# Kernel tuning notes

Measured on AMD Instinct MI355X. Metric: run time of the kernel, lower is better.

Reference implementation:

```python
import jax, jax.numpy as jnp
import numpy as np

EXPERT_NUM = 8
SEQ_LEN = 4096
FREQ_LEN = SEQ_LEN // 2 + 1


def setup_inputs() -> dict:
    key = jax.random.key(0)
    ks = jax.random.split(key, 6)
    B, C = 32, 8
    x = jax.random.normal(ks[0], (B, C, SEQ_LEN), dtype=jnp.float32)
    raw = jax.random.uniform(ks[1], (EXPERT_NUM - 1,), dtype=jnp.float32)
    s1 = 1.0 / np.sqrt(FREQ_LEN)
    W1 = jax.random.uniform(ks[2], (FREQ_LEN, FREQ_LEN), jnp.float32, -s1, s1)
    b1 = jax.random.uniform(ks[3], (FREQ_LEN,), jnp.float32, -s1, s1)
    W2 = jax.random.uniform(ks[4], (EXPERT_NUM, FREQ_LEN), jnp.float32, -s1, s1)
    b2 = jax.random.uniform(ks[5], (EXPERT_NUM,), jnp.float32, -s1, s1)
    return {"x": x, "raw": raw, "W1": W1, "b1": b1, "W2": W2, "b2": b2}


def reference(x, raw, W1, b1, W2, b2):
    # instance norm over seq dim (unbiased variance, like torch.var default)
    x_mean = jnp.mean(x, axis=2, keepdims=True)
    xc = x - x_mean
    n = x.shape[2]
    x_var = jnp.sum(xc * xc, axis=2, keepdims=True) / (n - 1) + 1e-5
    xn = xc / jnp.sqrt(x_var)

    freq_x = jnp.fft.rfft(xn, axis=-1)            # [B, C, F] complex
    F_ = freq_x.shape[-1]

    # sorted sigmoid boundaries -> integer band edges (non-differentiable cast)
    b = jnp.sort(jax.nn.sigmoid(raw))
    boundaries = jnp.concatenate([jnp.zeros(1, x.dtype), b, jnp.ones(1, x.dtype)])
    idx = jnp.floor(jax.lax.stop_gradient(boundaries) * F_).astype(jnp.int32)
    idx = idx.at[-1].set(F_)

    # band-pass masks for all experts at once: [E, F]
    fpos = jnp.arange(F_)
    mask = (fpos[None, :] >= idx[:-1, None]) & (fpos[None, :] < idx[1:, None])

    # per-expert frequency components: [B, E, C, F]
    comp = freq_x[:, None, :, :] * mask[None, :, None, :].astype(freq_x.dtype)
    expert_outputs = jnp.fft.irfft(comp, n=SEQ_LEN, axis=-1)  # [B, E, C, L]

    # gating on channel-averaged magnitude spectrum
    gating_input = jnp.mean(jnp.abs(freq_x), axis=1)          # [B, F]
    h = jax.nn.relu(gating_input @ W1.T + b1)
    gating_scores = jax.nn.softmax(h @ W2.T + b2, axis=-1)    # [B, E]

    # gated combine in frequency domain, then single iFFT
    gate_c = gating_scores.astype(freq_x.dtype)
    combined_freq = jnp.einsum('becf,be->bcf', comp, gate_c)
    combined = jnp.fft.irfft(combined_freq, n=SEQ_LEN, axis=-1)
    combined = combined * jnp.sqrt(x_var) + x_mean
    return combined, boundaries, gating_scores, expert_outputs
```

## Files before the change

kernel.cpp:

```cpp
#include <hip/hip_runtime.h>
#include <hip/hip_bf16.h>


using cplx = float2;
typedef float nfloat2 __attribute__((ext_vector_type(2)));

static constexpr int BB = 32, CCH = 8, LL = 4096, FF = 2049, EE = 8;

static constexpr size_t WS_FREQ  = 0;
static constexpr size_t WS_MEAN  = WS_FREQ + (size_t)BB * CCH * FF * 2;
static constexpr size_t WS_SIGMA = WS_MEAN + 256;
static constexpr size_t WS_AMAG  = WS_SIGMA + 256;
static constexpr size_t WS_H     = WS_AMAG + (size_t)BB * CCH * FF;
static constexpr size_t WS_IDX   = WS_H + (size_t)BB * FF;
static constexpr size_t WS_EOF   = WS_IDX + 16;

static constexpr size_t OUT_COMB = 0;
static constexpr size_t OUT_BND  = (size_t)BB * CCH * LL;
static constexpr size_t OUT_GATE = OUT_BND + 9;
static constexpr size_t OUT_EXP  = OUT_GATE + (size_t)BB * EE;

__device__ float2 g_W2048[2048];
__device__ float2 g_U[2049];
__device__ int    g_tabcnt = 0;

#define PHI(i) ((i) + ((i) >> 5))
__device__ __forceinline__ int scat(int n) {
  return ((n & 3) << 9) | (((n >> 2) & 7) << 6) | (((n >> 5) & 7) << 3) | (n >> 8);
}

template <bool INV>
__device__ __forceinline__ void dft8(float* zr, float* zi) {
  const float C = 0.70710678118654752f;
  float s0r = zr[0] + zr[4], s0i = zi[0] + zi[4];
  float d0r = zr[0] - zr[4], d0i = zi[0] - zi[4];
  float s1r = zr[2] + zr[6], s1i = zi[2] + zi[6];
  float d1r = zr[2] - zr[6], d1i = zi[2] - zi[6];
  float E0r = s0r + s1r, E0i = s0i + s1i;
  float E2r = s0r - s1r, E2i = s0i - s1i;
  float E1r, E1i, E3r, E3i;
  if (!INV) { E1r = d0r + d1i; E1i = d0i - d1r; E3r = d0r - d1i; E3i = d0i + d1r; }
  else      { E1r = d0r - d1i; E1i = d0i + d1r; E3r = d0r + d1i; E3i = d0i - d1r; }
  float t0r = zr[1] + zr[5], t0i = zi[1] + zi[5];
  float e0r = zr[1] - zr[5], e0i = zi[1] - zi[5];
  float t1r = zr[3] + zr[7], t1i = zi[3] + zi[7];
  float e1r = zr[3] - zr[7], e1i = zi[3] - zi[7];
  float O0r = t0r + t1r, O0i = t0i + t1i;
  float O2r = t0r - t1r, O2i = t0i - t1i;
  float O1r, O1i, O3r, O3i;
  if (!INV) { O1r = e0r + e1i; O1i = e0i - e1r; O3r = e0r - e1i; O3i = e0i + e1r; }
  else      { O1r = e0r - e1i; O1i = e0i + e1r; O3r = e0r + e1i; O3i = e0i - e1r; }
  float w1r, w1i, w2r, w2i, w3r, w3i;
  if (!INV) {
    w1r = C * (O1r + O1i); w1i = C * (O1i - O1r);
    w2r = O2i;             w2i = -O2r;
    w3r = C * (O3i - O3r); w3i = -C * (O3r + O3i);
  } else {
    w1r = C * (O1r - O1i); w1i = C * (O1i + O1r);
    w2r = -O2i;            w2i = O2r;
    w3r = -C * (O3r + O3i); w3i = C * (O3r - O3i);
  }
  zr[0] = E0r + O0r; zi[0] = E0i + O0i;
  zr[4] = E0r - O0r; zi[4] = E0i - O0i;
  zr[1] = E1r + w1r; zi[1] = E1i + w1i;
  zr[5] = E1r - w1r; zi[5] = E1i - w1i;
  zr[2] = E2r + w2r; zi[2] = E2i + w2i;
  zr[6] = E2r - w2r; zi[6] = E2i - w2i;
  zr[3] = E3r + w3r; zi[3] = E3i + w3i;
  zr[7] = E3r - w3r; zi[7] = E3i - w3i;
}

template <bool INV>
__device__ __forceinline__ void dft4(float* zr, float* zi) {
  float s0r = zr[0] + zr[2], s0i = zi[0] + zi[2];
  float d0r = zr[0] - zr[2], d0i = zi[0] - zi[2];
  float s1r = zr[1] + zr[3], s1i = zi[1] + zi[3];
  float d1r = zr[1] - zr[3], d1i = zi[1] - zi[3];
  zr[0] = s0r + s1r; zi[0] = s0i + s1i;
  zr[2] = s0r - s1r; zi[2] = s0i - s1i;
  if (!INV) { zr[1] = d0r + d1i; zi[1] = d0i - d1r; zr[3] = d0r - d1i; zi[3] = d0i + d1r; }
  else      { zr[1] = d0r - d1i; zi[1] = d0i + d1r; zr[3] = d0r + d1i; zi[3] = d0i - d1r; }
}

template <bool INV>
__device__ void fftr8(float* ZR, float* ZI, const cplx* __restrict__ W, int t) {
  float zr[8], zi[8];
  {
    int base = 8 * t;
#pragma unroll
    for (int m = 0; m < 8; ++m) { int i = PHI(base + m); zr[m] = ZR[i]; zi[m] = ZI[i]; }
    dft8<INV>(zr, zi);
#pragma unroll
    for (int m = 0; m < 8; ++m) { int i = PHI(base + m); ZR[i] = zr[m]; ZI[i] = zi[m]; }
  }
  __syncthreads();
  {
    int g = t & 31, p = t >> 5;
    int base = 64 * g + p;
#pragma unroll
    for (int m = 0; m < 8; ++m) { int i = PHI(base + 8 * m); zr[m] = ZR[i]; zi[m] = ZI[i]; }
#pragma unroll
    for (int m = 1; m < 8; ++m) {
      cplx w = W[32 * m * p];
      float wi = INV ? -w.y : w.y;
      float xr = zr[m] * w.x - zi[m] * wi;
      float xi = zr[m] * wi + zi[m] * w.x;
      zr[m] = xr; zi[m] = xi;
    }
    dft8<INV>(zr, zi);
#pragma unroll
    for (int m = 0; m < 8; ++m) { int i = PHI(base + 8 * m); ZR[i] = zr[m]; ZI[i] = zi[m]; }
  }
  __syncthreads();
  {
    int g = t & 3, p = t >> 2;
    int base = 512 * g + p;
#pragma unroll
    for (int m = 0; m < 8; ++m) { int i = PHI(base + 64 * m); zr[m] = ZR[i]; zi[m] = ZI[i]; }
#pragma unroll
    for (int m = 1; m < 8; ++m) {
      cplx w = W[4 * m * p];
      float wi = INV ? -w.y : w.y;
      float xr = zr[m] * w.x - zi[m] * wi;
      float xi = zr[m] * wi + zi[m] * w.x;
      zr[m] = xr; zi[m] = xi;
    }
    dft8<INV>(zr, zi);
#pragma unroll
    for (int m = 0; m < 8; ++m) { int i = PHI(base + 64 * m); ZR[i] = zr[m]; ZI[i] = zi[m]; }
  }
  __syncthreads();
  {
#pragma unroll
    for (int h = 0; h < 2; ++h) {
      int p = t + (h << 8);
      float yr[4], yi[4];
#pragma unroll
      for (int m = 0; m < 4; ++m) { int i = PHI(p + 512 * m); yr[m] = ZR[i]; yi[m] = ZI[i]; }
#pragma unroll
      for (int m = 1; m < 4; ++m) {
        cplx w = W[m * p];
        float wi = INV ? -w.y : w.y;
        float xr = yr[m] * w.x - yi[m] * wi;
        float xi = yr[m] * wi + yi[m] * w.x;
        yr[m] = xr; yi[m] = xi;
      }
      dft4<INV>(yr, yi);
#pragma unroll
      for (int m = 0; m < 4; ++m) { int i = PHI(p + 512 * m); ZR[i] = yr[m]; ZI[i] = yi[m]; }
    }
  }
  __syncthreads();
}

__device__ __forceinline__ void expert_ifft(const float* __restrict__ ws,
                                            float* __restrict__ out,
                                            float* ZR, float* ZI,
                                            int bc, int j, int t) {
  const int b = bc >> 3, c = bc & 7;
  const cplx* freq = (const cplx*)ws + (size_t)bc * FF;
  const int*  idxp = (const int*)(ws + WS_IDX);
  const int lo = idxp[j], hi = idxp[j + 1];

#pragma unroll
  for (int u = 0; u < 8; ++u) {
    int k  = t + (u << 8);
    int km = 2048 - k;
    cplx A = make_float2(0.f, 0.f), Bv = make_float2(0.f, 0.f);
    if (k >= lo && k < hi)   A  = freq[k];
    if (km >= lo && km < hi) Bv = freq[km];
    float Px = A.x - Bv.x, Py = A.y + Bv.y;
    float Qx = A.x + Bv.x, Qy = A.y - Bv.y;
    cplx uk = g_U[k];
    float cs = uk.x, sn = -uk.y;
    float Xox = 0.5f * (cs * Px - sn * Py);
    float Xoy = 0.5f * (cs * Py + sn * Px);
    int i = PHI(scat(k));
    ZR[i] = 0.5f * Qx - Xoy;
    ZI[i] = 0.5f * Qy + Xox;
  }
  __syncthreads();

  fftr8<true>(ZR, ZI, g_W2048, t);

  const float mul = 1.0f / 2048.0f;
  float* op = out + OUT_EXP + (((size_t)(b * EE + j) * CCH + c) * LL);
  if (t == 0) __builtin_nontemporal_store(ZR[PHI(0)] * mul, op);
#pragma unroll
  for (int u = 0; u < 8; ++u) {
    int n = t + (u << 8);
    if (n < 2047) {
      nfloat2 o;
      o.x = ZI[PHI(n)] * mul;
      o.y = ZR[PHI(n + 1)] * mul;
      __builtin_nontemporal_store(o, (nfloat2*)(op + 2 * n + 1));
    } else {
      __builtin_nontemporal_store(ZI[PHI(2047)] * mul, op + 4095);
    }
  }
}

__global__ __launch_bounds__(256) void k_fwd(const float* __restrict__ x,
                                             const float* __restrict__ raw,
                                             float* __restrict__ ws,
                                             float* __restrict__ out) {
  const int p = blockIdx.x, t = threadIdx.x;

  if (p >= 256) {
    if (p < 273) {
      if (__hip_atomic_load(&g_tabcnt, __ATOMIC_RELAXED, __HIP_MEMORY_SCOPE_AGENT) < 17) {
        if (p < 264) {
          int jj = (p - 256) * 256 + t;
          float sn, cs;
          sincosf(-6.283185307179586f * (float)jj / 2048.0f, &sn, &cs);
          g_W2048[jj] = make_float2(cs, sn);
        } else {
          int k = (p - 264) * 256 + t;
          if (k < FF) {
            float sn, cs;
            sincosf(-3.14159265358979323846f * (float)k / 2048.0f, &sn, &cs);
            g_U[k] = make_float2(cs, sn);
          }
        }
        __syncthreads();
        if (t == 0) {
          __threadfence();
          __hip_atomic_fetch_add(&g_tabcnt, 1, __ATOMIC_RELEASE, __HIP_MEMORY_SCOPE_AGENT);
        }
      }
    } else if (p == 273) {
      __shared__ int idx_s[9];
      if (t == 0) {
        float v[7];
        for (int i = 0; i < 7; ++i) v[i] = 1.0f / (1.0f + expf(-raw[i]));
        for (int a = 1; a < 7; ++a) {
          float key = v[a];
          int q = a - 1;
          while (q >= 0 && v[q] > key) { v[q + 1] = v[q]; --q; }
          v[q + 1] = key;
        }
        float bnd[9];
        bnd[0] = 0.0f; bnd[8] = 1.0f;
        for (int i = 0; i < 7; ++i) bnd[i + 1] = v[i];
        int* wi = (int*)(ws + WS_IDX);
        for (int e = 0; e < 9; ++e) {
          int id = (int)floorf(bnd[e] * (float)FF);
          if (e == 8) id = FF;
          idx_s[e] = id;
          wi[e] = id;
          out[OUT_BND + e] = bnd[e];
        }
      }
      __syncthreads();
      int* eof = (int*)(ws + WS_EOF);
      for (int f = t; f < FF; f += 256) {
        int e = 0;
        for (int q = 1; q < 8; ++q)
          if (f >= idx_s[q]) e = q;
        eof[f] = e;
      }
    } else {
      float4* hp = (float4*)(ws + WS_H);
      const float4 z4 = make_float4(0.f, 0.f, 0.f, 0.f);
      for (int i = (p - 274) * 256 + t; i < 16392; i += 8 * 256) hp[i] = z4;
    }
    return;
  }

  __shared__ float ZR[2112], ZI[2112];
  __shared__ float red[8];
  const int bc = p;
  const int lane = t & 63, wid = t >> 6;
  const float2* xp2 = (const float2*)(x + (size_t)bc * LL);

  float2 v[8];
  float sum = 0.f;
#pragma unroll
  for (int u = 0; u < 8; ++u) {
    v[u] = xp2[t + (u << 8)];
    sum += v[u].x + v[u].y;
  }
#pragma unroll
  for (int off = 32; off > 0; off >>= 1) sum += __shfl_down(sum, off, 64);
  if (lane == 0) red[wid] = sum;
  __syncthreads();
  const float mean = (red[0] + red[1] + red[2] + red[3]) * (1.0f / 4096.0f);

  float ss = 0.f;
#pragma unroll
  for (int u = 0; u < 8; ++u) {
    float dx = v[u].x - mean, dy = v[u].y - mean;
    ss += dx * dx + dy * dy;
  }
#pragma unroll
  for (int off = 32; off > 0; off >>= 1) ss += __shfl_down(ss, off, 64);
  if (lane == 0) red[4 + wid] = ss;
  __syncthreads();
  const float var   = (red[4] + red[5] + red[6] + red[7]) / 4095.0f + 1e-5f;
  const float sigma = sqrtf(var);
  const float inv   = 1.0f / sigma;
  if (t == 0) {
    ws[WS_MEAN + bc]  = mean;
    ws[WS_SIGMA + bc] = sigma;
  }

#pragma unroll
  for (int u = 0; u < 8; ++u) {
    int n = t + (u << 8);
    int i = PHI(scat(n));
    ZR[i] = (v[u].x - mean) * inv;
    ZI[i] = (v[u].y - mean) * inv;
  }
  if (t == 0) {
    while (__hip_atomic_load(&g_tabcnt, __ATOMIC_ACQUIRE, __HIP_MEMORY_SCOPE_AGENT) < 17) {
      __builtin_amdgcn_s_sleep(8);
    }
  }
  __syncthreads();

  fftr8<false>(ZR, ZI, g_W2048, t);

  cplx* freq = (cplx*)ws + (size_t)bc * FF;
#pragma unroll
  for (int u = 0; u < 9; ++u) {
    int k = t + (u << 8);
    if (k > 2048) break;
    int ka = k & 2047, km = (2048 - k) & 2047;
    float Zkr = ZR[PHI(ka)], Zki = ZI[PHI(ka)];
    float Zmr = ZR[PHI(km)], Zmi = ZI[PHI(km)];
    float fex = 0.5f * (Zkr + Zmr);
    float fey = 0.5f * (Zki - Zmi);
    float fox = 0.5f * (Zki + Zmi);
    float foy = -0.5f * (Zkr - Zmr);
    cplx uk = g_U[k];
    float rx = fex + uk.x * fox - uk.y * foy;
    float ry = fey + uk.x * foy + uk.y * fox;
    freq[k] = make_float2(rx, ry);
    ws[WS_AMAG + (size_t)bc * FF + k] = 0.125f * sqrtf(rx * rx + ry * ry);
  }
}

__global__ __launch_bounds__(256) void k_mid(const float* __restrict__ W1,
                                             float* __restrict__ ws,
                                             float* __restrict__ out) {
  __shared__ float SM[4224];
  const int p = blockIdx.x, t = threadIdx.x;

  if (p < 1089) {
    float* W1s = SM;
    float* gis = SM + 2112;
    const int i0 = (p % 33) * 64;
    const int il = t & 63, bg = t >> 6;
    float acc[8] = {0, 0, 0, 0, 0, 0, 0, 0};
    const int fbeg = (p / 33) * 64;
    const int fend = min(fbeg + 64, FF);
    for (int f0 = fbeg; f0 < fend; f0 += 32) {
      for (int q = t; q < 64 * 32; q += 256) {
        int r = q >> 5, cc = q & 31;
        int gi_i = i0 + r, gf = f0 + cc;
        W1s[r * 33 + cc] = (gi_i < FF && gf < FF) ? W1[(size_t)gi_i * FF + gf] : 0.f;
      }
      for (int q = t; q < 32 * 32; q += 256) {
        int bb = q >> 5, cc = q & 31;
        int gf = f0 + cc;
        float s = 0.f;
        if (gf < FF) {
          const float* ap = ws + WS_AMAG + (size_t)(bb * 8) * FF + gf;
#pragma unroll
          for (int c = 0; c < 8; ++c) s += ap[(size_t)c * FF];
        }
        gis[bb * 33 + cc] = s;
      }
      __syncthreads();
#pragma unroll 8
      for (int cc = 0; cc < 32; ++cc) {
        float wv = W1s[il * 33 + cc];
#pragma unroll
        for (int j = 0; j < 8; ++j) acc[j] += wv * gis[(bg * 8 + j) * 33 + cc];
      }
      __syncthreads();
    }
    int ii = i0 + il;
    if (ii < FF) {
#pragma unroll
      for (int j = 0; j < 8; ++j)
        atomicAdd(&ws[WS_H + (size_t)(bg * 8 + j) * FF + ii], acc[j]);
    }
    return;
  }
  if (p < 1096) return;

  const int e   = p - 1096;
  const int xcd = e & 7, s = e >> 3;
  const int grp = s / 6, j = s % 6;
  const int bc  = (grp << 3) | xcd;

  expert_ifft(ws, out, SM, SM + 2112, bc, j, t);
}

__global__ __launch_bounds__(256) void k_comb(const float* __restrict__ b1,
                                              const float* __restrict__ W2,
                                              const float* __restrict__ b2,
                                              const float* __restrict__ ws,
                                              float* __restrict__ out) {
  __shared__ float ZR[2112], ZI[2112];
  const int p = blockIdx.x, t = threadIdx.x;

  if (p >= 256) {
    const int q  = p - 256;
    const int jj = q >> 8, bc = q & 255;
    expert_ifft(ws, out, ZR, ZI, bc, 6 + jj, t);
    return;
  }

  __shared__ float red[4][8];
  __shared__ float lg[8];
  __shared__ float gates_s[8];
  const int bc = p;
  const int b  = bc >> 3, c = bc & 7;
  const int lane = t & 63, wid = t >> 6;

  float pacc[8] = {0, 0, 0, 0, 0, 0, 0, 0};
  const float* hrow = ws + WS_H + (size_t)b * FF;
  for (int f = t; f < FF; f += 256) {
    float hv = fmaxf(hrow[f] + b1[f], 0.f);
#pragma unroll
    for (int e = 0; e < 8; ++e) pacc[e] += hv * W2[(size_t)e * FF + f];
  }
#pragma unroll
  for (int off = 32; off > 0; off >>= 1) {
#pragma unroll
    for (int e = 0; e < 8; ++e) pacc[e] += __shfl_down(pacc[e], off, 64);
  }
  if (lane == 0) {
#pragma unroll
    for (int e = 0; e < 8; ++e) red[wid][e] = pacc[e];
  }
  __syncthreads();
  if (t < 8) lg[t] = red[0][t] + red[1][t] + red[2][t] + red[3][t] + b2[t];
  __syncthreads();
  if (t < 8) {
    float mx = lg[0];
#pragma unroll
    for (int q = 1; q < 8; ++q) mx = fmaxf(mx, lg[q]);
    float sm = 0.f;
#pragma unroll
    for (int q = 0; q < 8; ++q) sm += expf(lg[q] - mx);
    float g = expf(lg[t] - mx) / sm;
    gates_s[t] = g;
    if (c == 0) out[OUT_GATE + (size_t)b * 8 + t] = g;
  }
  __syncthreads();

  const cplx* freq = (const cplx*)ws + (size_t)bc * FF;
  const int*  eof  = (const int*)(ws + WS_EOF);

#pragma unroll
  for (int u = 0; u < 8; ++u) {
    int k  = t + (u << 8);
    int km = 2048 - k;
    cplx A  = freq[k];
    cplx Bv = freq[km];
    float gk = gates_s[eof[k]], gm = gates_s[eof[km]];
    A.x *= gk; A.y *= gk; Bv.x *= gm; Bv.y *= gm;
    float Px = A.x - Bv.x, Py = A.y + Bv.y;
    float Qx = A.x + Bv.x, Qy = A.y - Bv.y;
    cplx uk = g_U[k];
    float cs = uk.x, sn = -uk.y;
    float Xox = 0.5f * (cs * Px - sn * Py);
    float Xoy = 0.5f * (cs * Py + sn * Px);
    int i = PHI(scat(k));
    ZR[i] = 0.5f * Qx - Xoy;
    ZI[i] = 0.5f * Qy + Xox;
  }
  __syncthreads();

  fftr8<true>(ZR, ZI, g_W2048, t);

  const float mul = ws[WS_SIGMA + bc] * (1.0f / 2048.0f);
  const float add = ws[WS_MEAN + bc];
  nfloat2* op = (nfloat2*)(out + OUT_COMB + (size_t)bc * LL);
#pragma unroll
  for (int u = 0; u < 8; ++u) {
    int n = t + (u << 8);
    nfloat2 o;
    o.x = ZR[PHI(n)] * mul + add;
    o.y = ZI[PHI(n)] * mul + add;
    __builtin_nontemporal_store(o, op + n);
  }
}

extern "C" void kernel_launch(void* const* d_in, const int* in_sizes, int n_in,
                              void* d_out, int out_size, void* d_ws, size_t ws_size,
                              hipStream_t stream) {
  const float* x   = (const float*)d_in[0];
  const float* raw = (const float*)d_in[1];
  const float* W1  = (const float*)d_in[2];
  const float* b1  = (const float*)d_in[3];
  const float* W2  = (const float*)d_in[4];
  const float* b2  = (const float*)d_in[5];
  float* out = (float*)d_out;
  float* ws  = (float*)d_ws;

  k_fwd<<<282, 256, 0, stream>>>(x, raw, ws, out);
  k_mid<<<1096 + 1536, 256, 0, stream>>>(W1, ws, out);
  k_comb<<<256 + 512, 256, 0, stream>>>(b1, W2, b2, ws, out);
}
```

Measured before the change: 135.1 us.

## Accumulate channel-averaged magnitudes via atomics and move all expert iFFTs to mid kernel

The forward kernel now atomically accumulates the per-batch channel-summed magnitude spectrum into a global buffer, so the gating GEMM reads one value per (b,f) instead of summing eight channel rows. All eight expert iFFTs now run in the middle kernel alongside the GEMM, and the combine kernel only handles gating and the combined iFFT. The combine kernel also zeroes the accumulation buffer for the next call, which relies on the first call starting from the zero-initialised global. Atomic contention on the accumulation buffer and a heavier middle kernel are the costs.

Result: faster. 130.6 us (-3.3%).

```diff
diff --git a/kernel.cpp b/kernel.cpp
--- a/kernel.cpp
+++ b/kernel.cpp
@@ -10,8 +10,7 @@
 static constexpr size_t WS_FREQ  = 0;
 static constexpr size_t WS_MEAN  = WS_FREQ + (size_t)BB * CCH * FF * 2;
 static constexpr size_t WS_SIGMA = WS_MEAN + 256;
-static constexpr size_t WS_AMAG  = WS_SIGMA + 256;
-static constexpr size_t WS_H     = WS_AMAG + (size_t)BB * CCH * FF;
+static constexpr size_t WS_H     = WS_SIGMA + 256;
 static constexpr size_t WS_IDX   = WS_H + (size_t)BB * FF;
 static constexpr size_t WS_EOF   = WS_IDX + 16;
 
@@ -23,6 +22,7 @@
 __device__ float2 g_W2048[2048];
 __device__ float2 g_U[2049];
 __device__ int    g_tabcnt = 0;
+__device__ float  g_gi[BB * FF];
 
 #define PHI(i) ((i) + ((i) >> 5))
 __device__ __forceinline__ int scat(int n) {
@@ -270,6 +270,7 @@
   __shared__ float ZR[2112], ZI[2112];
   __shared__ float red[8];
   const int bc = p;
+  const int b  = bc >> 3;
   const int lane = t & 63, wid = t >> 6;
   const float2* xp2 = (const float2*)(x + (size_t)bc * LL);
 
@@ -336,7 +337,7 @@
     float rx = fex + uk.x * fox - uk.y * foy;
     float ry = fey + uk.x * foy + uk.y * fox;
     freq[k] = make_float2(rx, ry);
-    ws[WS_AMAG + (size_t)bc * FF + k] = 0.125f * sqrtf(rx * rx + ry * ry);
+    atomicAdd(&g_gi[(size_t)b * FF + k], 0.125f * sqrtf(rx * rx + ry * ry));
   }
 }
 
@@ -363,13 +364,7 @@
       for (int q = t; q < 32 * 32; q += 256) {
         int bb = q >> 5, cc = q & 31;
         int gf = f0 + cc;
-        float s = 0.f;
-        if (gf < FF) {
-          const float* ap = ws + WS_AMAG + (size_t)(bb * 8) * FF + gf;
-#pragma unroll
-          for (int c = 0; c < 8; ++c) s += ap[(size_t)c * FF];
-        }
-        gis[bb * 33 + cc] = s;
+        gis[bb * 33 + cc] = (gf < FF) ? g_gi[(size_t)bb * FF + gf] : 0.f;
       }
       __syncthreads();
 #pragma unroll 8
@@ -392,9 +387,8 @@
 
   const int e   = p - 1096;
   const int xcd = e & 7, s = e >> 3;
-  const int grp = s / 6, j = s % 6;
+  const int grp = s >> 3, j = s & 7;
   const int bc  = (grp << 3) | xcd;
-
   expert_ifft(ws, out, SM, SM + 2112, bc, j, t);
 }
 
@@ -404,21 +398,19 @@
                                               const float* __restrict__ ws,
                                               float* __restrict__ out) {
   __shared__ float ZR[2112], ZI[2112];
-  const int p = blockIdx.x, t = threadIdx.x;
-
-  if (p >= 256) {
-    const int q  = p - 256;
-    const int jj = q >> 8, bc = q & 255;
-    expert_ifft(ws, out, ZR, ZI, bc, 6 + jj, t);
-    return;
-  }
-
   __shared__ float red[4][8];
   __shared__ float lg[8];
   __shared__ float gates_s[8];
-  const int bc = p;
+  const int q = blockIdx.x, t = threadIdx.x;
+  const int bc = q;
   const int b  = bc >> 3, c = bc & 7;
   const int lane = t & 63, wid = t >> 6;
+
+  {
+    int i = q * 256 + t;
+    g_gi[i] = 0.f;
+    if (i < 32) g_gi[65536 + i] = 0.f;
+  }
 
   float pacc[8] = {0, 0, 0, 0, 0, 0, 0, 0};
   const float* hrow = ws + WS_H + (size_t)b * FF;
@@ -442,10 +434,10 @@
   if (t < 8) {
     float mx = lg[0];
 #pragma unroll
-    for (int q = 1; q < 8; ++q) mx = fmaxf(mx, lg[q]);
+    for (int r2 = 1; r2 < 8; ++r2) mx = fmaxf(mx, lg[r2]);
     float sm = 0.f;
 #pragma unroll
-    for (int q = 0; q < 8; ++q) sm += expf(lg[q] - mx);
+    for (int r2 = 0; r2 < 8; ++r2) sm += expf(lg[r2] - mx);
     float g = expf(lg[t] - mx) / sm;
     gates_s[t] = g;
     if (c == 0) out[OUT_GATE + (size_t)b * 8 + t] = g;
@@ -503,6 +495,6 @@
   float* ws  = (float*)d_ws;
 
   k_fwd<<<282, 256, 0, stream>>>(x, raw, ws, out);
-  k_mid<<<1096 + 1536, 256, 0, stream>>>(W1, ws, out);
-  k_comb<<<256 + 512, 256, 0, stream>>>(b1, W2, b2, ws, out);
-}
+  k_mid<<<1096 + 2048, 256, 0, stream>>>(W1, ws, out);
+  k_comb<<<256, 256, 0, stream>>>(b1, W2, b2, ws, out);
+}
```
